# Performance work log

Hardware: AMD Instinct MI355X
Metric: run time of the kernel (lower is better)

The kernel has to match this reference:

```python
import jax, jax.numpy as jnp
import numpy as np

N = 100000      # nodes (dtype==2 subgraph)
E = 1600000     # edges
IN_DIM = 256
OUT_DIM = 64
FEAT_DIM = 64   # hard-coded by nn.Linear(64, out_dim) in dstfeat_fc


def setup_inputs() -> dict:
    key = jax.random.key(0)
    k1, k2, k3, k4, k5, k6 = jax.random.split(key, 6)
    h = jax.random.normal(k1, (N, IN_DIM), dtype=jnp.float32)
    feat = jax.random.normal(k2, (N, FEAT_DIM), dtype=jnp.float32)
    W_fc = jax.random.normal(k3, (OUT_DIM, IN_DIM), dtype=jnp.float32) * 0.05
    W_dst = jax.random.normal(k4, (OUT_DIM, FEAT_DIM), dtype=jnp.float32) * 0.05
    src = jax.random.randint(k5, (E,), 0, N, dtype=jnp.int64)
    dst = jax.random.randint(k6, (E,), 0, N, dtype=jnp.int64)
    return {"h": h, "feat": feat, "W_fc": W_fc, "W_dst": W_dst, "src": src, "dst": dst}


def reference(h, feat, W_fc, W_dst, src, dst):
    # node projections (done once per node, then gathered per edge)
    z = h @ W_fc.T            # [N, OUT]  (self.fc)
    df = feat @ W_dst.T       # [N, OUT]  (self.dstfeat_fc on dst 'feat')

    # per-edge attention logit: dot(z[src], dstfeat[dst])
    e = jnp.sum(z[src] * df[dst], axis=-1)          # [E]

    # segment softmax over incoming edges of each destination node
    emax = jax.ops.segment_max(e, dst, num_segments=N)
    emax = jnp.where(jnp.isfinite(emax), emax, 0.0)  # guard empty segments
    ex = jnp.exp(e - emax[dst])                      # [E]
    denom = jax.ops.segment_sum(ex, dst, num_segments=N)  # [N]

    # weighted neighbor aggregation: sum_e alpha_e * z[src_e] per dst
    num = jax.ops.segment_sum(ex[:, None] * z[src], dst, num_segments=N)  # [N, OUT]
    out = num / jnp.where(denom == 0, 1.0, denom)[:, None]
    return out
```

## Files before the change

kernel.cpp:

```cpp
#include <hip/hip_runtime.h>
#include <math.h>

typedef unsigned int uint32;
typedef __attribute__((ext_vector_type(8))) short bf16x8;
typedef __attribute__((ext_vector_type(4))) float f32x4;

__device__ __forceinline__ ushort f2bf(float f) {
  uint32 u = __builtin_bit_cast(uint32, f);
  uint32 r = (u + 0x7fff + ((u >> 16) & 1)) >> 16;
  return (ushort)r;
}
__device__ __forceinline__ float bf_lo(uint32 u) {
  return __builtin_bit_cast(float, u << 16);
}
__device__ __forceinline__ float bf_hi(uint32 u) {
  return __builtin_bit_cast(float, u & 0xffff0000u);
}

#define NBBITS 8
#define BKNODES 256
#define CH 4096
#define NBMAX 512

template <int K, bool BF16OUT>
__device__ __forceinline__ void gemm_body(const float* __restrict__ A,
                                          const float* __restrict__ W,
                                          ushort* __restrict__ Cb,
                                          float* __restrict__ C,
                                          int M, int bx, ushort* Ws) {
  const int t = threadIdx.x;
  const int lane = t & 63;
  const int w = t >> 6;
  const int quad = lane >> 4;
  const int l16 = lane & 15;
  const int rBase = bx * 128;
  const int WSTR = K + 8;

  const int kq4 = K >> 2;
  for (int idx = t; idx < 64 * kq4; idx += 256) {
    int row = idx / kq4, kq = idx - row * kq4;
    float4 v = *(const float4*)(W + (size_t)row * K + kq * 4);
    ushort4 b;
    b.x = f2bf(v.x); b.y = f2bf(v.y); b.z = f2bf(v.z); b.w = f2bf(v.w);
    *(ushort4*)&Ws[row * WSTR + kq * 4] = b;
  }
  __syncthreads();

  f32x4 acc[2][4];
  #pragma unroll
  for (int i = 0; i < 2; ++i)
    #pragma unroll
    for (int n = 0; n < 4; ++n) acc[i][n] = (f32x4){0.f, 0.f, 0.f, 0.f};

  const int r0 = min(rBase + w * 32 + l16, M - 1);
  const int r1 = min(rBase + w * 32 + 16 + l16, M - 1);
  const float* __restrict__ a0 = A + (size_t)r0 * K + quad * 8;
  const float* __restrict__ a1 = A + (size_t)r1 * K + quad * 8;

  float4 c00 = *(const float4*)(a0);
  float4 c01 = *(const float4*)(a0 + 4);
  float4 c10 = *(const float4*)(a1);
  float4 c11 = *(const float4*)(a1 + 4);

  #pragma unroll 2
  for (int kb = 0; kb < K; kb += 32) {
    float4 n00, n01, n10, n11;
    const bool more = (kb + 32 < K);
    if (more) {
      n00 = *(const float4*)(a0 + kb + 32);
      n01 = *(const float4*)(a0 + kb + 36);
      n10 = *(const float4*)(a1 + kb + 32);
      n11 = *(const float4*)(a1 + kb + 36);
    }

    bf16x8 af0, af1;
    af0[0] = (short)f2bf(c00.x); af0[1] = (short)f2bf(c00.y);
    af0[2] = (short)f2bf(c00.z); af0[3] = (short)f2bf(c00.w);
    af0[4] = (short)f2bf(c01.x); af0[5] = (short)f2bf(c01.y);
    af0[6] = (short)f2bf(c01.z); af0[7] = (short)f2bf(c01.w);
    af1[0] = (short)f2bf(c10.x); af1[1] = (short)f2bf(c10.y);
    af1[2] = (short)f2bf(c10.z); af1[3] = (short)f2bf(c10.w);
    af1[4] = (short)f2bf(c11.x); af1[5] = (short)f2bf(c11.y);
    af1[6] = (short)f2bf(c11.z); af1[7] = (short)f2bf(c11.w);

    bf16x8 bfrag[4];
    #pragma unroll
    for (int n = 0; n < 4; ++n)
      bfrag[n] = *(const bf16x8*)&Ws[(n * 16 + l16) * WSTR + kb + quad * 8];

    #pragma unroll
    for (int n = 0; n < 4; ++n) {
      acc[0][n] = __builtin_amdgcn_mfma_f32_16x16x32_bf16(af0, bfrag[n], acc[0][n], 0, 0, 0);
      acc[1][n] = __builtin_amdgcn_mfma_f32_16x16x32_bf16(af1, bfrag[n], acc[1][n], 0, 0, 0);
    }

    if (more) { c00 = n00; c01 = n01; c10 = n10; c11 = n11; }
  }

  #pragma unroll
  for (int i = 0; i < 2; ++i)
    #pragma unroll
    for (int nt = 0; nt < 4; ++nt)
      #pragma unroll
      for (int r = 0; r < 4; ++r) {
        int row = rBase + w * 32 + i * 16 + quad * 4 + r;
        int col = nt * 16 + l16;
        if (row < M) {
          if (BF16OUT)
            Cb[(size_t)row * 64 + col] = f2bf(acc[i][nt][r]);
          else
            C[(size_t)row * 64 + col] = acc[i][nt][r];
        }
      }
}

__device__ __forceinline__ void count_body(const int* __restrict__ dst,
                                           int* __restrict__ bCnt,
                                           int E, int NB, int cb, int* lcnt) {
  const int t = threadIdx.x;
  for (int i = t; i < NB; i += 256) lcnt[i] = 0;
  __syncthreads();
  const int c0 = cb * CH, c1 = min(c0 + CH, E);
  for (int i = c0 + t; i < c1; i += 256) atomicAdd(&lcnt[dst[i] >> NBBITS], 1);
  __syncthreads();
  for (int b = t; b < NB; b += 256) {
    int c = lcnt[b];
    if (c) atomicAdd(&bCnt[b], c);
  }
}

__global__ __launch_bounds__(256, 4) void gemm_count(const float* __restrict__ h,
                                                     const float* __restrict__ feat,
                                                     const float* __restrict__ W_fc,
                                                     const float* __restrict__ W_dst,
                                                     ushort* __restrict__ zb,
                                                     float* __restrict__ df,
                                                     const int* __restrict__ dst,
                                                     int* __restrict__ bCnt,
                                                     int M, int gsplit, int E, int NB,
                                                     int nChunks) {
  __shared__ __align__(16) ushort Ws[64 * 264];
  const int bx = (int)blockIdx.x;
  if (bx < nChunks)
    count_body(dst, bCnt, E, NB, bx, (int*)Ws);
  else if (bx < nChunks + gsplit)
    gemm_body<256, true>(h, W_fc, zb, nullptr, M, bx - nChunks, Ws);
  else
    gemm_body<64, false>(feat, W_dst, nullptr, df, M, bx - nChunks - gsplit, Ws);
}

__device__ __forceinline__ void block_scan512(const int* __restrict__ bCnt,
                                              int NB, int* sc) {
  const int t = threadIdx.x;
  {
    int v0 = (t < NB) ? bCnt[t] : 0;
    int v1 = (t + 256 < NB) ? bCnt[t + 256] : 0;
    sc[t] = v0;
    sc[t + 256] = v1;
  }
  __syncthreads();
  for (int off = 1; off < NBMAX; off <<= 1) {
    int v0 = sc[t];
    int a0 = (t >= off) ? sc[t - off] : 0;
    int v1 = sc[t + 256];
    int a1 = sc[t + 256 - off];
    __syncthreads();
    sc[t] = v0 + a0;
    sc[t + 256] = v1 + a1;
    __syncthreads();
  }
}

__global__ __launch_bounds__(256) void csr_partition(const int* __restrict__ src,
                                                     const int* __restrict__ dst,
                                                     const int* __restrict__ bCnt,
                                                     int* __restrict__ relCur,
                                                     unsigned* __restrict__ packed,
                                                     int E, int NB) {
  __shared__ int sc[NBMAX];
  __shared__ int lcnt[NBMAX];
  __shared__ int lbase[NBMAX];
  const int t = threadIdx.x;
  block_scan512(bCnt, NB, sc);
  for (int i = t; i < NB; i += 256) lcnt[i] = 0;
  __syncthreads();
  const int c0 = blockIdx.x * CH, c1 = min(c0 + CH, E);
  for (int i = c0 + t; i < c1; i += 256) atomicAdd(&lcnt[dst[i] >> NBBITS], 1);
  __syncthreads();
  for (int b = t; b < NB; b += 256) {
    int c = lcnt[b];
    lbase[b] = c ? (sc[b] - bCnt[b] + atomicAdd(&relCur[b], c)) : 0;
  }
  __syncthreads();
  for (int i = c0 + t; i < c1; i += 256) {
    int dv = dst[i];
    int b = dv >> NBBITS;
    int pos = atomicAdd(&lbase[b], 1);
    packed[pos] = ((unsigned)src[i] << NBBITS) | (unsigned)(dv & (BKNODES - 1));
  }
}

__global__ __launch_bounds__(256) void csr_finalize(const int* __restrict__ bCnt,
                                                    const unsigned* __restrict__ packed,
                                                    int* __restrict__ edgeSrc,
                                                    int* __restrict__ offsets,
                                                    int N, int NB, int E) {
  __shared__ int sc[NBMAX];
  __shared__ int sh[BKNODES];
  __shared__ int wsum[4];
  const int r = blockIdx.x;
  const int t = threadIdx.x;
  const int lane = t & 63, wave = t >> 6;
  block_scan512(bCnt, NB, sc);
  const int endr = sc[r];
  const int base = endr - bCnt[r];
  __syncthreads();
  sh[t] = 0;
  __syncthreads();
  for (int i = base + t; i < endr; i += 256)
    atomicAdd(&sh[packed[i] & (BKNODES - 1)], 1);
  __syncthreads();
  {
    int x = sh[t];
    int inc = x;
    #pragma unroll
    for (int d = 1; d < 64; d <<= 1) {
      int o = __shfl_up(inc, d, 64);
      if (lane >= d) inc += o;
    }
    if (lane == 63) wsum[wave] = inc;
    __syncthreads();
    int wbase = 0;
    #pragma unroll
    for (int w = 0; w < 4; ++w)
      if (w < wave) wbase += wsum[w];
    int excl = wbase + inc - x;
    __syncthreads();
    sh[t] = base + excl;
  }
  __syncthreads();
  const int node0 = r << NBBITS;
  {
    int g = node0 + t;
    if (g < N) offsets[g] = sh[t];
  }
  if (r == NB - 1 && t == 0) offsets[N] = E;
  __syncthreads();
  for (int i = base + t; i < endr; i += 256) {
    unsigned v = packed[i];
    int pos = atomicAdd(&sh[v & (BKNODES - 1)], 1);
    edgeSrc[pos] = (int)(v >> NBBITS);
  }
}

__global__ __launch_bounds__(256) void aggregate(const ushort* __restrict__ zb,
                                                 const float* __restrict__ df,
                                                 const int* __restrict__ offsets,
                                                 const int* __restrict__ edgeSrc,
                                                 float* __restrict__ out, int N, int NW) {
  const int lane = threadIdx.x & 63;
  int d = __builtin_amdgcn_readfirstlane((int)((blockIdx.x * blockDim.x + threadIdx.x) >> 6));
  if (d >= N) return;
  const int g = lane >> 4;
  const int l16 = lane & 15;

  int beg = offsets[d];
  int end = offsets[d + 1];
  float4 df4 = *(const float4*)(df + (size_t)d * 64 + l16 * 4);

  while (true) {
    const int nd = d + NW;
    const int ndc = min(nd, N - 1);
    const int nbeg = offsets[ndc];
    const int nend = offsets[ndc + 1];
    const float4 ndf4 = *(const float4*)(df + (size_t)ndc * 64 + l16 * 4);

    float m = -INFINITY, l = 0.f;
    float ax = 0.f, ay = 0.f, az = 0.f, aw = 0.f;

    for (int j0 = beg; j0 < end; j0 += 32) {
      const int nst = min(8, (end - j0 + 3) >> 2);
      uint2 zf[8];
      float ew[8];
      float bm = -INFINITY;

      #pragma unroll
      for (int st = 0; st < 8; ++st) {
        if (st < nst) {
          const int eidx = j0 + st * 4 + g;
          const bool act = eidx < end;
          int s = 0;
          if (act) s = edgeSrc[eidx];
          zf[st] = *(const uint2*)(zb + (size_t)s * 64 + l16 * 4);
          float p = bf_lo(zf[st].x) * df4.x;
          p = fmaf(bf_hi(zf[st].x), df4.y, p);
          p = fmaf(bf_lo(zf[st].y), df4.z, p);
          p = fmaf(bf_hi(zf[st].y), df4.w, p);
          p += __shfl_xor(p, 1, 64);
          p += __shfl_xor(p, 2, 64);
          p += __shfl_xor(p, 4, 64);
          p += __shfl_xor(p, 8, 64);
          ew[st] = act ? p : -INFINITY;
          bm = fmaxf(bm, ew[st]);
        }
      }
      bm = fmaxf(bm, __shfl_xor(bm, 16, 64));
      bm = fmaxf(bm, __shfl_xor(bm, 32, 64));

      const float nm = fmaxf(m, bm);
      const float alpha = __expf(m - nm);
      float sw = 0.f;
      #pragma unroll
      for (int st = 0; st < 8; ++st) {
        if (st < nst) {
          const float w = __expf(ew[st] - nm);
          ew[st] = w;
          sw += w;
        }
      }
      sw += __shfl_xor(sw, 16, 64);
      sw += __shfl_xor(sw, 32, 64);
      l = l * alpha + sw;
      m = nm;

      ax *= alpha; ay *= alpha; az *= alpha; aw *= alpha;
      #pragma unroll
      for (int st = 0; st < 8; ++st) {
        if (st < nst) {
          const float w = ew[st];
          ax = fmaf(w, bf_lo(zf[st].x), ax);
          ay = fmaf(w, bf_hi(zf[st].x), ay);
          az = fmaf(w, bf_lo(zf[st].y), az);
          aw = fmaf(w, bf_hi(zf[st].y), aw);
        }
      }
    }

    ax += __shfl_xor(ax, 16, 64); ax += __shfl_xor(ax, 32, 64);
    ay += __shfl_xor(ay, 16, 64); ay += __shfl_xor(ay, 32, 64);
    az += __shfl_xor(az, 16, 64); az += __shfl_xor(az, 32, 64);
    aw += __shfl_xor(aw, 16, 64); aw += __shfl_xor(aw, 32, 64);

    if (lane < 16) {
      const float inv = (l > 0.f) ? (1.f / l) : 0.f;
      float4 o;
      o.x = ax * inv; o.y = ay * inv; o.z = az * inv; o.w = aw * inv;
      *(float4*)(out + (size_t)d * 64 + l16 * 4) = o;
    }

    if (nd >= N) break;
    d = nd; beg = nbeg; end = nend; df4 = ndf4;
  }
}

extern "C" void kernel_launch(void* const* d_in, const int* in_sizes, int n_in,
                              void* d_out, int out_size, void* d_ws, size_t ws_size,
                              hipStream_t stream) {
  const float* h     = (const float*)d_in[0];
  const float* feat  = (const float*)d_in[1];
  const float* W_fc  = (const float*)d_in[2];
  const float* W_dst = (const float*)d_in[3];
  const int*   src   = (const int*)d_in[4];
  const int*   dst   = (const int*)d_in[5];
  float* out = (float*)d_out;

  const int N = in_sizes[1] / 64;
  const int E = in_sizes[4];

  const int NB = (N + BKNODES - 1) >> NBBITS;
  const int nChunks = (E + CH - 1) / CH;

  char* ws = (char*)d_ws;
  ushort* zb = (ushort*)ws;
  float* df = (float*)(zb + (size_t)N * 64);
  int* offsets = (int*)(df + (size_t)N * 64);
  int* edgeSrc = offsets + N + 1;
  int* bCnt = edgeSrc + E;
  int* relCur = bCnt + NB;
  unsigned* packed = (unsigned*)d_out;

  hipMemsetAsync(bCnt, 0, sizeof(int) * (size_t)(2 * NB), stream);

  const int gsplit = (N + 127) / 128;
  gemm_count<<<nChunks + gsplit * 2, 256, 0, stream>>>(h, feat, W_fc, W_dst, zb, df,
                                                       dst, bCnt, N, gsplit, E, NB,
                                                       nChunks);

  csr_partition<<<nChunks, 256, 0, stream>>>(src, dst, bCnt, relCur, packed, E, NB);
  csr_finalize<<<NB, 256, 0, stream>>>(bCnt, packed, edgeSrc, offsets, N, NB, E);

  const int aggBlocks = 2048;
  const int NW = aggBlocks * 4;
  aggregate<<<aggBlocks, 256, 0, stream>>>(zb, df, offsets, edgeSrc, out, N, NW);
}
```

Measured before the change: 328.7 us.

## Pre-convert weights to bf16 in a prep kernel and widen CSR kernels to 512 threads

Adds a small prep kernel that converts both weight matrices to bf16 once and zeroes the bucket counters, replacing the memset. The GEMM blocks now read weight fragments straight from global memory instead of converting them into shared memory per block, which frees LDS so more blocks can fit per CU. The CSR partition and finalize kernels move to 512-thread blocks with a simpler one-element-per-thread scan. Loading weights from global memory adds cache traffic, and the log-step scan in finalize uses more barriers than the old shuffle-based scan.

```diff
diff --git a/kernel.cpp b/kernel.cpp
--- a/kernel.cpp
+++ b/kernel.cpp
@@ -22,29 +22,40 @@
 #define CH 4096
 #define NBMAX 512
 
+__global__ __launch_bounds__(256) void prep(const float* __restrict__ W_fc,
+                                            const float* __restrict__ W_dst,
+                                            ushort* __restrict__ Wb_fc,
+                                            ushort* __restrict__ Wb_dst,
+                                            int* __restrict__ zeroBuf, int nZero) {
+  const int tid = blockIdx.x * 256 + threadIdx.x;
+  const int stride = gridDim.x * 256;
+  for (int i = tid; i < (64 * 256) / 4; i += stride) {
+    float4 v = ((const float4*)W_fc)[i];
+    ushort4 b;
+    b.x = f2bf(v.x); b.y = f2bf(v.y); b.z = f2bf(v.z); b.w = f2bf(v.w);
+    ((ushort4*)Wb_fc)[i] = b;
+  }
+  for (int i = tid; i < (64 * 64) / 4; i += stride) {
+    float4 v = ((const float4*)W_dst)[i];
+    ushort4 b;
+    b.x = f2bf(v.x); b.y = f2bf(v.y); b.z = f2bf(v.z); b.w = f2bf(v.w);
+    ((ushort4*)Wb_dst)[i] = b;
+  }
+  for (int i = tid; i < nZero; i += stride) zeroBuf[i] = 0;
+}
+
 template <int K, bool BF16OUT>
 __device__ __forceinline__ void gemm_body(const float* __restrict__ A,
-                                          const float* __restrict__ W,
+                                          const ushort* __restrict__ Wb,
                                           ushort* __restrict__ Cb,
                                           float* __restrict__ C,
-                                          int M, int bx, ushort* Ws) {
+                                          int M, int bx) {
   const int t = threadIdx.x;
   const int lane = t & 63;
   const int w = t >> 6;
   const int quad = lane >> 4;
   const int l16 = lane & 15;
   const int rBase = bx * 128;
-  const int WSTR = K + 8;
-
-  const int kq4 = K >> 2;
-  for (int idx = t; idx < 64 * kq4; idx += 256) {
-    int row = idx / kq4, kq = idx - row * kq4;
-    float4 v = *(const float4*)(W + (size_t)row * K + kq * 4);
-    ushort4 b;
-    b.x = f2bf(v.x); b.y = f2bf(v.y); b.z = f2bf(v.z); b.w = f2bf(v.w);
-    *(ushort4*)&Ws[row * WSTR + kq * 4] = b;
-  }
-  __syncthreads();
 
   f32x4 acc[2][4];
   #pragma unroll
@@ -86,7 +97,7 @@
     bf16x8 bfrag[4];
     #pragma unroll
     for (int n = 0; n < 4; ++n)
-      bfrag[n] = *(const bf16x8*)&Ws[(n * 16 + l16) * WSTR + kb + quad * 8];
+      bfrag[n] = *(const bf16x8*)(Wb + (size_t)(n * 16 + l16) * K + kb + quad * 8);
 
     #pragma unroll
     for (int n = 0; n < 4; ++n) {
@@ -131,47 +142,39 @@
 
 __global__ __launch_bounds__(256, 4) void gemm_count(const float* __restrict__ h,
                                                      const float* __restrict__ feat,
-                                                     const float* __restrict__ W_fc,
-                                                     const float* __restrict__ W_dst,
+                                                     const ushort* __restrict__ Wb_fc,
+                                                     const ushort* __restrict__ Wb_dst,
                                                      ushort* __restrict__ zb,
                                                      float* __restrict__ df,
                                                      const int* __restrict__ dst,
                                                      int* __restrict__ bCnt,
                                                      int M, int gsplit, int E, int NB,
                                                      int nChunks) {
-  __shared__ __align__(16) ushort Ws[64 * 264];
+  __shared__ int lcnt[NBMAX];
   const int bx = (int)blockIdx.x;
   if (bx < nChunks)
-    count_body(dst, bCnt, E, NB, bx, (int*)Ws);
+    count_body(dst, bCnt, E, NB, bx, lcnt);
   else if (bx < nChunks + gsplit)
-    gemm_body<256, true>(h, W_fc, zb, nullptr, M, bx - nChunks, Ws);
+    gemm_body<256, true>(h, Wb_fc, zb, nullptr, M, bx - nChunks);
   else
-    gemm_body<64, false>(feat, W_dst, nullptr, df, M, bx - nChunks - gsplit, Ws);
-}
-
-__device__ __forceinline__ void block_scan512(const int* __restrict__ bCnt,
-                                              int NB, int* sc) {
-  const int t = threadIdx.x;
-  {
-    int v0 = (t < NB) ? bCnt[t] : 0;
-    int v1 = (t + 256 < NB) ? bCnt[t + 256] : 0;
-    sc[t] = v0;
-    sc[t + 256] = v1;
-  }
+    gemm_body<64, false>(feat, Wb_dst, nullptr, df, M, bx - nChunks - gsplit);
+}
+
+__device__ __forceinline__ void scan512w(const int* __restrict__ bCnt, int NB,
+                                         int* sc) {
+  const int t = threadIdx.x;
+  sc[t] = (t < NB) ? bCnt[t] : 0;
   __syncthreads();
   for (int off = 1; off < NBMAX; off <<= 1) {
-    int v0 = sc[t];
-    int a0 = (t >= off) ? sc[t - off] : 0;
-    int v1 = sc[t + 256];
-    int a1 = sc[t + 256 - off];
+    int v = sc[t];
+    int a = (t >= off) ? sc[t - off] : 0;
     __syncthreads();
-    sc[t] = v0 + a0;
-    sc[t + 256] = v1 + a1;
+    sc[t] = v + a;
     __syncthreads();
   }
 }
 
-__global__ __launch_bounds__(256) void csr_partition(const int* __restrict__ src,
+__global__ __launch_bounds__(512) void csr_partition(const int* __restrict__ src,
                                                      const int* __restrict__ dst,
                                                      const int* __restrict__ bCnt,
                                                      int* __restrict__ relCur,
@@ -181,18 +184,18 @@
   __shared__ int lcnt[NBMAX];
   __shared__ int lbase[NBMAX];
   const int t = threadIdx.x;
-  block_scan512(bCnt, NB, sc);
-  for (int i = t; i < NB; i += 256) lcnt[i] = 0;
+  scan512w(bCnt, NB, sc);
+  lcnt[t] = 0;
   __syncthreads();
   const int c0 = blockIdx.x * CH, c1 = min(c0 + CH, E);
-  for (int i = c0 + t; i < c1; i += 256) atomicAdd(&lcnt[dst[i] >> NBBITS], 1);
-  __syncthreads();
-  for (int b = t; b < NB; b += 256) {
-    int c = lcnt[b];
-    lbase[b] = c ? (sc[b] - bCnt[b] + atomicAdd(&relCur[b], c)) : 0;
-  }
-  __syncthreads();
-  for (int i = c0 + t; i < c1; i += 256) {
+  for (int i = c0 + t; i < c1; i += 512) atomicAdd(&lcnt[dst[i] >> NBBITS], 1);
+  __syncthreads();
+  if (t < NB) {
+    int c = lcnt[t];
+    lbase[t] = c ? (sc[t] - bCnt[t] + atomicAdd(&relCur[t], c)) : 0;
+  }
+  __syncthreads();
+  for (int i = c0 + t; i < c1; i += 512) {
     int dv = dst[i];
     int b = dv >> NBBITS;
     int pos = atomicAdd(&lbase[b], 1);
@@ -200,53 +203,41 @@
   }
 }
 
-__global__ __launch_bounds__(256) void csr_finalize(const int* __restrict__ bCnt,
+__global__ __launch_bounds__(512) void csr_finalize(const int* __restrict__ bCnt,
                                                     const unsigned* __restrict__ packed,
                                                     int* __restrict__ edgeSrc,
                                                     int* __restrict__ offsets,
                                                     int N, int NB, int E) {
   __shared__ int sc[NBMAX];
   __shared__ int sh[BKNODES];
-  __shared__ int wsum[4];
   const int r = blockIdx.x;
   const int t = threadIdx.x;
-  const int lane = t & 63, wave = t >> 6;
-  block_scan512(bCnt, NB, sc);
+  scan512w(bCnt, NB, sc);
   const int endr = sc[r];
   const int base = endr - bCnt[r];
-  __syncthreads();
-  sh[t] = 0;
-  __syncthreads();
-  for (int i = base + t; i < endr; i += 256)
+  if (t < BKNODES) sh[t] = 0;
+  __syncthreads();
+  for (int i = base + t; i < endr; i += 512)
     atomicAdd(&sh[packed[i] & (BKNODES - 1)], 1);
   __syncthreads();
-  {
-    int x = sh[t];
-    int inc = x;
-    #pragma unroll
-    for (int d = 1; d < 64; d <<= 1) {
-      int o = __shfl_up(inc, d, 64);
-      if (lane >= d) inc += o;
-    }
-    if (lane == 63) wsum[wave] = inc;
+  const int cnt_t = (t < BKNODES) ? sh[t] : 0;
+  for (int off = 1; off < BKNODES; off <<= 1) {
+    int v = 0;
+    if (t < BKNODES) v = sh[t] + ((t >= off) ? sh[t - off] : 0);
     __syncthreads();
-    int wbase = 0;
-    #pragma unroll
-    for (int w = 0; w < 4; ++w)
-      if (w < wave) wbase += wsum[w];
-    int excl = wbase + inc - x;
+    if (t < BKNODES) sh[t] = v;
     __syncthreads();
-    sh[t] = base + excl;
-  }
+  }
+  if (t < BKNODES) sh[t] = base + sh[t] - cnt_t;
   __syncthreads();
   const int node0 = r << NBBITS;
-  {
+  if (t < BKNODES) {
     int g = node0 + t;
     if (g < N) offsets[g] = sh[t];
   }
   if (r == NB - 1 && t == 0) offsets[N] = E;
   __syncthreads();
-  for (int i = base + t; i < endr; i += 256) {
+  for (int i = base + t; i < endr; i += 512) {
     unsigned v = packed[i];
     int pos = atomicAdd(&sh[v & (BKNODES - 1)], 1);
     edgeSrc[pos] = (int)(v >> NBBITS);
@@ -371,7 +362,9 @@
   const int nChunks = (E + CH - 1) / CH;
 
   char* ws = (char*)d_ws;
-  ushort* zb = (ushort*)ws;
+  ushort* Wb_fc = (ushort*)ws;
+  ushort* Wb_dst = Wb_fc + 64 * 256;
+  ushort* zb = Wb_dst + 64 * 64;
   float* df = (float*)(zb + (size_t)N * 64);
   int* offsets = (int*)(df + (size_t)N * 64);
   int* edgeSrc = offsets + N + 1;
@@ -379,15 +372,15 @@
   int* relCur = bCnt + NB;
   unsigned* packed = (unsigned*)d_out;
 
-  hipMemsetAsync(bCnt, 0, sizeof(int) * (size_t)(2 * NB), stream);
+  prep<<<32, 256, 0, stream>>>(W_fc, W_dst, Wb_fc, Wb_dst, bCnt, 2 * NB);
 
   const int gsplit = (N + 127) / 128;
-  gemm_count<<<nChunks + gsplit * 2, 256, 0, stream>>>(h, feat, W_fc, W_dst, zb, df,
+  gemm_count<<<nChunks + gsplit * 2, 256, 0, stream>>>(h, feat, Wb_fc, Wb_dst, zb, df,
                                                        dst, bCnt, N, gsplit, E, NB,
                                                        nChunks);
 
-  csr_partition<<<nChunks, 256, 0, stream>>>(src, dst, bCnt, relCur, packed, E, NB);
-  csr_finalize<<<NB, 256, 0, stream>>>(bCnt, packed, edgeSrc, offsets, N, NB, E);
+  csr_partition<<<nChunks, 512, 0, stream>>>(src, dst, bCnt, relCur, packed, E, NB);
+  csr_finalize<<<NB, 512, 0, stream>>>(bCnt, packed, edgeSrc, offsets, N, NB, E);
 
   const int aggBlocks = 2048;
   const int NW = aggBlocks * 4;
```

Result: no change. 331.1 us (+0.7%).
